# Kernel tuning notes

Measured on AMD Instinct MI355X. Metric: run time of the kernel, lower is better.

Reference implementation:

```python
import jax, jax.numpy as jnp
import numpy as np

N, C, K = 800_000, 64, 27  # active voxels, channels, 3^3 kernel offsets
EPS = 1e-5  # MinkowskiBatchNorm default eps


def setup_inputs() -> dict:
    key = jax.random.key(0)
    ks = jax.random.split(key, 9)
    x = jax.random.normal(ks[0], (N, C), jnp.float32)
    nbr = jax.random.randint(ks[1], (N, K), 0, N, jnp.int32)        # kernel-map input indices
    mask_bits = jax.random.randint(ks[2], (N, K), 0, 2, jnp.int32)
    W1 = jax.random.normal(ks[3], (K, C, C), jnp.float32) * 0.05    # conv1 weights (bias=False in ME)
    W2 = jax.random.normal(ks[4], (K, C, C), jnp.float32) * 0.05    # conv2 weights
    g1 = jax.random.normal(ks[5], (C,), jnp.float32) * 0.1 + 1.0
    b1 = jax.random.normal(ks[6], (C,), jnp.float32) * 0.1
    g2 = jax.random.normal(ks[7], (C,), jnp.float32) * 0.1 + 1.0
    b2 = jax.random.normal(ks[8], (C,), jnp.float32) * 0.1
    return {"x": x, "nbr": nbr, "mask_bits": mask_bits,
            "W1": W1, "g1": g1, "b1": b1, "W2": W2, "g2": g2, "b2": b2}


def _bn(h, gamma, beta):
    # training-mode BatchNorm over the point dimension (biased variance, as torch BN)
    mean = h.mean(axis=0)
    var = ((h - mean) ** 2).mean(axis=0)
    return (h - mean) * jax.lax.rsqrt(var + EPS) * gamma + beta


def _sparse_conv(h, nbr, mask, W):
    # gather-GEMM-scatter sparse conv: out[n] = sum_k mask[n,k] * h[nbr[n,k]] @ W[k]
    out0 = jnp.zeros((h.shape[0], W.shape[2]), h.dtype)

    def body(acc, kin):
        w_k, n_k, m_k = kin  # [C,C], [N], [N]
        acc = acc + (h[n_k] * m_k[:, None]) @ w_k
        return acc, None

    out, _ = jax.lax.scan(body, out0, (W, nbr.T, mask.T))
    return out


def reference(x, nbr, mask_bits, W1, g1, b1, W2, g2, b2):
    mask = mask_bits.astype(x.dtype)
    identity = x  # shortcut is identity: stride=1 and in_channels == out_channels
    out = jax.nn.relu(_bn(_sparse_conv(x, nbr, mask, W1), g1, b1))
    out = _bn(_sparse_conv(out, nbr, mask, W2), g2, b2)
    return jax.nn.relu(out + identity)
```

## Files before the change

### kernel.cpp

```cpp
#include <hip/hip_runtime.h>

typedef unsigned short u16;
typedef unsigned int u32;
typedef __bf16 bf16x8 __attribute__((ext_vector_type(8)));
typedef u16 u16x8 __attribute__((ext_vector_type(8)));
typedef float f32x4 __attribute__((ext_vector_type(4)));

#define KOFF 27
#define KPAD 28
#define EPSV 1e-5f
#define FRAGS_PER_CONV 14336
#define LDS_S 133

__device__ __forceinline__ u16 f2bf(float f) {
  u32 u = __builtin_bit_cast(u32, f);
  u = (u + 0x7FFFu + ((u >> 16) & 1u)) >> 16;
  return (u16)u;
}
__device__ __forceinline__ float bf2f(u16 h) {
  return __builtin_bit_cast(float, (u32)h << 16);
}

__device__ __forceinline__ void gl_lds16(const void* g, void* l) {
  __builtin_amdgcn_global_load_lds(
      (__attribute__((address_space(1))) void*)g,
      (__attribute__((address_space(3))) void*)l, 16, 0, 0);
}

__global__ void prep_x(const float* __restrict__ x, u16* __restrict__ xg, int n8) {
  int stride = gridDim.x * blockDim.x;
  for (int i = blockIdx.x * blockDim.x + threadIdx.x; i < n8; i += stride) {
    const f32x4* p = reinterpret_cast<const f32x4*>(x) + i * 2;
    f32x4 v0 = p[0], v1 = p[1];
    u16x8 o;
    o[0] = f2bf(v0[0]); o[1] = f2bf(v0[1]); o[2] = f2bf(v0[2]); o[3] = f2bf(v0[3]);
    o[4] = f2bf(v1[0]); o[5] = f2bf(v1[1]); o[6] = f2bf(v1[2]); o[7] = f2bf(v1[3]);
    reinterpret_cast<u16x8*>(xg)[i] = o;
  }
}

__global__ __launch_bounds__(256) void prep_tcidx(
    const int* __restrict__ nbr, const int* __restrict__ msk,
    int* __restrict__ cidx_q) {
  __shared__ int lds[27 * LDS_S + 16];
  const int tid = threadIdx.x;
  const int blk = blockIdx.x;
  const int in_base = blk * (128 * KOFF);
#pragma unroll
  for (int it = 0; it < 14; it++) {
    int t = tid + it * 256;
    if (t < 128 * KOFF) {
      int g = in_base + t;
      int v = msk[g] ? nbr[g] : -1;
      int row = (u32)t / KOFF;
      int k = t - row * KOFF;
      lds[k * LDS_S + row] = v;
    }
  }
  __syncthreads();
  const int out_base = blk * (2 * KPAD * 64);
#pragma unroll
  for (int it = 0; it < 14; it++) {
    int o = tid + it * 256;
    int q = (u32)o / (KPAD * 64);
    int rem = o - q * (KPAD * 64);
    int k = rem >> 6;
    int sub = rem & 63;
    int r = sub >> 2;
    int j = sub & 3;
    int v = (k < KOFF) ? lds[k * LDS_S + q * 64 + j * 16 + r] : -1;
    cidx_q[out_base + o] = v;
  }
}

__global__ void prep_w(const float* __restrict__ W1, const float* __restrict__ W2,
                       u16* __restrict__ wf) {
  int tid = blockIdx.x * blockDim.x + threadIdx.x;
  if (tid >= 2 * FRAGS_PER_CONV) return;
  int conv = tid / FRAGS_PER_CONV;
  int slot = tid - conv * FRAGS_PER_CONV;
  int k = slot >> 9;
  u16x8 o;
  if (k >= KOFF) {
#pragma unroll
    for (int j = 0; j < 8; j++) o[j] = 0;
  } else {
    const float* src = conv ? W2 : W1;
    int rest = slot & 511;
    int c = rest >> 8;
    int nt = (rest >> 6) & 3;
    int lane = rest & 63;
    int col = nt * 16 + (lane & 15);
    int kk0 = c * 32 + (lane >> 4) * 8;
    int base = k * 4096 + kk0 * 64 + col;
#pragma unroll
    for (int j = 0; j < 8; j++) o[j] = f2bf(src[base + j * 64]);
  }
  reinterpret_cast<u16x8*>(wf)[tid] = o;
}

__global__ __launch_bounds__(256, 4) void sconv(
    const u16* __restrict__ xg, const int* __restrict__ cidx_q,
    const u16* __restrict__ wf, u16* __restrict__ hout,
    float* __restrict__ psum, float* __restrict__ psq) {
  __shared__ __align__(1024) bf16x8 bsm[2][512];
  const int lane = threadIdx.x & 63;
  const int r = lane & 15;
  const int kg = lane >> 4;
  const int widInBlk = threadIdx.x >> 6;
  const int waveId = blockIdx.x * 4 + widInBlk;
  const char* wfc = (const char*)wf;
  const int chOff = kg * 8;
  bf16x8 zz;
#pragma unroll
  for (int j = 0; j < 8; j++) zz[j] = (__bf16)0.0f;

  const int n0 = waveId * 64;
  const int4* cpq = reinterpret_cast<const int4*>(cidx_q) +
                    (size_t)waveId * (KPAD * 16) + r;

  f32x4 acc[4][4];
#pragma unroll
  for (int j = 0; j < 4; j++)
#pragma unroll
    for (int nt = 0; nt < 4; nt++) {
      acc[j][nt][0] = 0.f; acc[j][nt][1] = 0.f;
      acc[j][nt][2] = 0.f; acc[j][nt][3] = 0.f;
    }

#define STAGEB(bc, ks)                                                     \
  {                                                                        \
    const char* s = wfc + ((size_t)(ks) << 13) + widInBlk * 1024 + lane * 16; \
    char* d = (char*)&bsm[bc][0] + widInBlk * 1024 + lane * 16;            \
    gl_lds16(s, d);                                                        \
    gl_lds16(s + 4096, d + 4096);                                          \
  }

  STAGEB(0, 0);

  for (int k = 0; k < KOFF; k++) {
    asm volatile("s_waitcnt vmcnt(0)" ::: "memory");
    __syncthreads();
    if (k + 1 < KOFF) STAGEB((k + 1) & 1, k + 1);

    int4 id4 = cpq[k << 4];
    bf16x8 a0[4], a1[4];
#pragma unroll
    for (int j = 0; j < 4; j++) { a0[j] = zz; a1[j] = zz; }
    if (id4.x >= 0) {
      const bf16x8* ap = reinterpret_cast<const bf16x8*>(xg + ((size_t)id4.x << 6) + chOff);
      a0[0] = ap[0]; a1[0] = ap[4];
    }
    if (id4.y >= 0) {
      const bf16x8* ap = reinterpret_cast<const bf16x8*>(xg + ((size_t)id4.y << 6) + chOff);
      a0[1] = ap[0]; a1[1] = ap[4];
    }
    if (id4.z >= 0) {
      const bf16x8* ap = reinterpret_cast<const bf16x8*>(xg + ((size_t)id4.z << 6) + chOff);
      a0[2] = ap[0]; a1[2] = ap[4];
    }
    if (id4.w >= 0) {
      const bf16x8* ap = reinterpret_cast<const bf16x8*>(xg + ((size_t)id4.w << 6) + chOff);
      a0[3] = ap[0]; a1[3] = ap[4];
    }
    const bf16x8* bl = &bsm[k & 1][0];
#pragma unroll
    for (int nt = 0; nt < 4; nt++) {
      bf16x8 b = bl[nt * 64 + lane];
#pragma unroll
      for (int j = 0; j < 4; j++)
        acc[j][nt] = __builtin_amdgcn_mfma_f32_16x16x32_bf16(a0[j], b, acc[j][nt], 0, 0, 0);
    }
#pragma unroll
    for (int nt = 0; nt < 4; nt++) {
      bf16x8 b = bl[256 + nt * 64 + lane];
#pragma unroll
      for (int j = 0; j < 4; j++)
        acc[j][nt] = __builtin_amdgcn_mfma_f32_16x16x32_bf16(a1[j], b, acc[j][nt], 0, 0, 0);
    }
  }
#undef STAGEB

  float ssum[4] = {0.f, 0.f, 0.f, 0.f};
  float ssq[4] = {0.f, 0.f, 0.f, 0.f};
#pragma unroll
  for (int j = 0; j < 4; j++) {
#pragma unroll
    for (int nt = 0; nt < 4; nt++) {
      const int col = nt * 16 + r;
      float rs = 0.f, rq = 0.f;
#pragma unroll
      for (int reg = 0; reg < 4; reg++) {
        float v = acc[j][nt][reg];
        rs += v;
        rq += v * v;
        hout[(size_t)(n0 + j * 16 + kg * 4 + reg) * 64 + col] = f2bf(v);
      }
      ssum[nt] += rs;
      ssq[nt] += rq;
    }
  }
#pragma unroll
  for (int nt = 0; nt < 4; nt++) {
    ssum[nt] += __shfl_xor(ssum[nt], 16, 64);
    ssum[nt] += __shfl_xor(ssum[nt], 32, 64);
    ssq[nt] += __shfl_xor(ssq[nt], 16, 64);
    ssq[nt] += __shfl_xor(ssq[nt], 32, 64);
  }
  if (lane < 16) {
#pragma unroll
    for (int nt = 0; nt < 4; nt++) {
      psum[(size_t)waveId * 64 + nt * 16 + lane] = ssum[nt];
      psq[(size_t)waveId * 64 + nt * 16 + lane] = ssq[nt];
    }
  }
}

__global__ void bn_finalize(const float* __restrict__ psum, const float* __restrict__ psq,
                            const float* __restrict__ g, const float* __restrict__ b,
                            float* __restrict__ scale, float* __restrict__ shift,
                            float invN, int nw) {
  int c = blockIdx.x;
  float s = 0.f, q = 0.f;
  for (int i = threadIdx.x; i < nw; i += blockDim.x) {
    s += psum[(size_t)i * 64 + c];
    q += psq[(size_t)i * 64 + c];
  }
#pragma unroll
  for (int off = 32; off >= 1; off >>= 1) {
    s += __shfl_down(s, off, 64);
    q += __shfl_down(q, off, 64);
  }
  __shared__ float ls[4], lq[4];
  int wid = threadIdx.x >> 6;
  int lane = threadIdx.x & 63;
  if (lane == 0) { ls[wid] = s; lq[wid] = q; }
  __syncthreads();
  if (threadIdx.x == 0) {
    s = ls[0] + ls[1] + ls[2] + ls[3];
    q = lq[0] + lq[1] + lq[2] + lq[3];
    float mean = s * invN;
    float var = q * invN - mean * mean;
    float rstd = rsqrtf(var + EPSV);
    float sc = rstd * g[c];
    scale[c] = sc;
    shift[c] = b[c] - mean * sc;
  }
}

__global__ void bn_relu_apply(const u16* __restrict__ h, const float* __restrict__ scale,
                              const float* __restrict__ shift, u16* __restrict__ y, int n8) {
  int i0 = blockIdx.x * blockDim.x + threadIdx.x;
  int c0 = (i0 * 8) & 63;
  float sc[8], sh[8];
#pragma unroll
  for (int j = 0; j < 8; j++) { sc[j] = scale[c0 + j]; sh[j] = shift[c0 + j]; }
  int stride = gridDim.x * blockDim.x;
  for (int i = i0; i < n8; i += stride) {
    u16x8 hv = reinterpret_cast<const u16x8*>(h)[i];
    u16x8 o;
#pragma unroll
    for (int j = 0; j < 8; j++) {
      float f = bf2f(hv[j]) * sc[j] + sh[j];
      o[j] = f2bf(fmaxf(f, 0.f));
    }
    reinterpret_cast<u16x8*>(y)[i] = o;
  }
}

__global__ void bn_add_relu(const u16* __restrict__ h, const float* __restrict__ scale,
                            const float* __restrict__ shift, const u16* __restrict__ xg,
                            float* __restrict__ out, int n8) {
  int i0 = blockIdx.x * blockDim.x + threadIdx.x;
  int c0 = (i0 * 8) & 63;
  float sc[8], sh[8];
#pragma unroll
  for (int j = 0; j < 8; j++) { sc[j] = scale[c0 + j]; sh[j] = shift[c0 + j]; }
  int stride = gridDim.x * blockDim.x;
  for (int i = i0; i < n8; i += stride) {
    u16x8 hv = reinterpret_cast<const u16x8*>(h)[i];
    u16x8 xv = reinterpret_cast<const u16x8*>(xg)[i];
    f32x4 o0, o1;
#pragma unroll
    for (int j = 0; j < 4; j++) {
      o0[j] = fmaxf(bf2f(hv[j]) * sc[j] + sh[j] + bf2f(xv[j]), 0.f);
      o1[j] = fmaxf(bf2f(hv[j + 4]) * sc[j + 4] + sh[j + 4] + bf2f(xv[j + 4]), 0.f);
    }
    f32x4* op = reinterpret_cast<f32x4*>(out) + i * 2;
    op[0] = o0;
    op[1] = o1;
  }
}

extern "C" void kernel_launch(void* const* d_in, const int* in_sizes, int n_in,
                              void* d_out, int out_size, void* d_ws, size_t ws_size,
                              hipStream_t stream) {
  const float* x = (const float*)d_in[0];
  const int* nbr = (const int*)d_in[1];
  const int* msk = (const int*)d_in[2];
  const float* W1 = (const float*)d_in[3];
  const float* g1 = (const float*)d_in[4];
  const float* b1 = (const float*)d_in[5];
  const float* W2 = (const float*)d_in[6];
  const float* g2 = (const float*)d_in[7];
  const float* b2 = (const float*)d_in[8];
  float* out = (float*)d_out;

  const int N = in_sizes[0] / 64;
  const int nquads = N / 64;
  const int nblocks = nquads / 4;
  const int n8 = N * 8;
  const size_t NC2 = (size_t)N * 64 * 2;
  const size_t MAPB = NC2 + 256;

  char* ws = (char*)d_ws;
  u16* bufA = (u16*)ws;
  u16* bufB = (u16*)(ws + MAPB);
  u16* wf = (u16*)(ws + 2 * MAPB);
  float* psum = (float*)(ws + 2 * MAPB + 512 * 1024);
  float* psq = psum + (size_t)nquads * 64;
  float* sc = psq + (size_t)nquads * 64;

  int* cidx_q = (int*)d_out;
  u16* y1 = (u16*)((char*)d_out + (size_t)N * KPAD * 4);

  float invN = 1.0f / (float)N;

  prep_x<<<2048, 256, 0, stream>>>(x, bufA, n8);
  prep_tcidx<<<N / 128, 256, 0, stream>>>(nbr, msk, cidx_q);
  prep_w<<<112, 256, 0, stream>>>(W1, W2, wf);
  sconv<<<nblocks, 256, 0, stream>>>(bufA, cidx_q, wf, bufB, psum, psq);
  bn_finalize<<<64, 256, 0, stream>>>(psum, psq, g1, b1, sc, sc + 64, invN, nquads);
  bn_relu_apply<<<2048, 256, 0, stream>>>(bufB, sc, sc + 64, y1, n8);
  sconv<<<nblocks, 256, 0, stream>>>(y1, cidx_q, wf + FRAGS_PER_CONV * 8, bufB, psum, psq);
  bn_finalize<<<64, 256, 0, stream>>>(psum, psq, g2, b2, sc + 128, sc + 192, invN, nquads);
  bn_add_relu<<<2048, 256, 0, stream>>>(bufB, sc + 128, sc + 192, bufA, out, n8);
}
```

Baseline: 841.1 us.

## Stage three kernel offsets per barrier with 512-thread sconv blocks

The sparse-conv kernel now uses 8-wave blocks and stages three offsets' weight fragments (24 KB) into LDS per phase, so the loop runs 10 barrier phases instead of 27. Weight fragments are padded to 30 slots and the grid is rounded up to whole 8-wave blocks. Waves past the last real row group still join the barriers but skip compute and write zero partial sums. The aim is to cut barrier and wait overhead per offset. In exchange the kernel uses more LDS per block, which may lower occupancy, and the padded waves do idle work.

```diff
diff --git a/kernel.cpp b/kernel.cpp
--- a/kernel.cpp
+++ b/kernel.cpp
@@ -8,8 +8,9 @@
 
 #define KOFF 27
 #define KPAD 28
+#define KSLOT 30
 #define EPSV 1e-5f
-#define FRAGS_PER_CONV 14336
+#define FRAGS_PER_CONV 15360
 #define LDS_S 133
 
 __device__ __forceinline__ u16 f2bf(float f) {
@@ -99,16 +100,17 @@
   reinterpret_cast<u16x8*>(wf)[tid] = o;
 }
 
-__global__ __launch_bounds__(256, 4) void sconv(
+__global__ __launch_bounds__(512, 4) void sconv(
     const u16* __restrict__ xg, const int* __restrict__ cidx_q,
     const u16* __restrict__ wf, u16* __restrict__ hout,
-    float* __restrict__ psum, float* __restrict__ psq) {
-  __shared__ __align__(1024) bf16x8 bsm[2][512];
+    float* __restrict__ psum, float* __restrict__ psq, int nquadsActive) {
+  __shared__ __align__(1024) bf16x8 bsm[2][1536];
   const int lane = threadIdx.x & 63;
   const int r = lane & 15;
   const int kg = lane >> 4;
   const int widInBlk = threadIdx.x >> 6;
-  const int waveId = blockIdx.x * 4 + widInBlk;
+  const int waveId = blockIdx.x * 8 + widInBlk;
+  const bool active = waveId < nquadsActive;
   const char* wfc = (const char*)wf;
   const int chOff = kg * 8;
   bf16x8 zz;
@@ -128,76 +130,85 @@
       acc[j][nt][2] = 0.f; acc[j][nt][3] = 0.f;
     }
 
-#define STAGEB(bc, ks)                                                     \
-  {                                                                        \
-    const char* s = wfc + ((size_t)(ks) << 13) + widInBlk * 1024 + lane * 16; \
-    char* d = (char*)&bsm[bc][0] + widInBlk * 1024 + lane * 16;            \
-    gl_lds16(s, d);                                                        \
-    gl_lds16(s + 4096, d + 4096);                                          \
-  }
-
-  STAGEB(0, 0);
-
-  for (int k = 0; k < KOFF; k++) {
+#define STAGE3(bc, ph)                                                        \
+  {                                                                           \
+    const char* s = wfc + (((size_t)(ph) * 3) << 13) + widInBlk * 1024 + lane * 16; \
+    char* d = (char*)&bsm[bc][0] + widInBlk * 1024 + lane * 16;               \
+    gl_lds16(s, d);                                                           \
+    gl_lds16(s + 8192, d + 8192);                                             \
+    gl_lds16(s + 16384, d + 16384);                                           \
+  }
+
+#define KSECT(K, bl)                                                          \
+  {                                                                           \
+    int4 id4 = cpq[(K) << 4];                                                 \
+    bf16x8 a0[4], a1[4];                                                      \
+    _Pragma("unroll") for (int j = 0; j < 4; j++) { a0[j] = zz; a1[j] = zz; } \
+    if (id4.x >= 0) {                                                         \
+      const bf16x8* ap = reinterpret_cast<const bf16x8*>(xg + ((size_t)id4.x << 6) + chOff); \
+      a0[0] = ap[0]; a1[0] = ap[4];                                           \
+    }                                                                         \
+    if (id4.y >= 0) {                                                         \
+      const bf16x8* ap = reinterpret_cast<const bf16x8*>(xg + ((size_t)id4.y << 6) + chOff); \
+      a0[1] = ap[0]; a1[1] = ap[4];                                           \
+    }                                                                         \
+    if (id4.z >= 0) {                                                         \
+      const bf16x8* ap = reinterpret_cast<const bf16x8*>(xg + ((size_t)id4.z << 6) + chOff); \
+      a0[2] = ap[0]; a1[2] = ap[4];                                           \
+    }                                                                         \
+    if (id4.w >= 0) {                                                         \
+      const bf16x8* ap = reinterpret_cast<const bf16x8*>(xg + ((size_t)id4.w << 6) + chOff); \
+      a0[3] = ap[0]; a1[3] = ap[4];                                           \
+    }                                                                         \
+    _Pragma("unroll") for (int nt = 0; nt < 4; nt++) {                        \
+      bf16x8 b = (bl)[nt * 64 + lane];                                        \
+      _Pragma("unroll") for (int j = 0; j < 4; j++)                           \
+        acc[j][nt] = __builtin_amdgcn_mfma_f32_16x16x32_bf16(a0[j], b, acc[j][nt], 0, 0, 0); \
+    }                                                                         \
+    _Pragma("unroll") for (int nt = 0; nt < 4; nt++) {                        \
+      bf16x8 b = (bl)[256 + nt * 64 + lane];                                  \
+      _Pragma("unroll") for (int j = 0; j < 4; j++)                           \
+        acc[j][nt] = __builtin_amdgcn_mfma_f32_16x16x32_bf16(a1[j], b, acc[j][nt], 0, 0, 0); \
+    }                                                                         \
+  }
+
+  STAGE3(0, 0);
+
+  for (int t = 0; t < 10; t++) {
     asm volatile("s_waitcnt vmcnt(0)" ::: "memory");
     __syncthreads();
-    if (k + 1 < KOFF) STAGEB((k + 1) & 1, k + 1);
-
-    int4 id4 = cpq[k << 4];
-    bf16x8 a0[4], a1[4];
-#pragma unroll
-    for (int j = 0; j < 4; j++) { a0[j] = zz; a1[j] = zz; }
-    if (id4.x >= 0) {
-      const bf16x8* ap = reinterpret_cast<const bf16x8*>(xg + ((size_t)id4.x << 6) + chOff);
-      a0[0] = ap[0]; a1[0] = ap[4];
-    }
-    if (id4.y >= 0) {
-      const bf16x8* ap = reinterpret_cast<const bf16x8*>(xg + ((size_t)id4.y << 6) + chOff);
-      a0[1] = ap[0]; a1[1] = ap[4];
-    }
-    if (id4.z >= 0) {
-      const bf16x8* ap = reinterpret_cast<const bf16x8*>(xg + ((size_t)id4.z << 6) + chOff);
-      a0[2] = ap[0]; a1[2] = ap[4];
-    }
-    if (id4.w >= 0) {
-      const bf16x8* ap = reinterpret_cast<const bf16x8*>(xg + ((size_t)id4.w << 6) + chOff);
-      a0[3] = ap[0]; a1[3] = ap[4];
-    }
-    const bf16x8* bl = &bsm[k & 1][0];
-#pragma unroll
-    for (int nt = 0; nt < 4; nt++) {
-      bf16x8 b = bl[nt * 64 + lane];
-#pragma unroll
-      for (int j = 0; j < 4; j++)
-        acc[j][nt] = __builtin_amdgcn_mfma_f32_16x16x32_bf16(a0[j], b, acc[j][nt], 0, 0, 0);
-    }
-#pragma unroll
-    for (int nt = 0; nt < 4; nt++) {
-      bf16x8 b = bl[256 + nt * 64 + lane];
-#pragma unroll
-      for (int j = 0; j < 4; j++)
-        acc[j][nt] = __builtin_amdgcn_mfma_f32_16x16x32_bf16(a1[j], b, acc[j][nt], 0, 0, 0);
-    }
-  }
-#undef STAGEB
+    if (t + 1 < 10) STAGE3((t + 1) & 1, t + 1);
+
+    if (active) {
+      const bf16x8* bl = &bsm[t & 1][0];
+      const int k0 = 3 * t;
+      KSECT(k0, bl);
+      if (k0 + 1 < KPAD) KSECT(k0 + 1, bl + 512);
+      if (k0 + 2 < KPAD) KSECT(k0 + 2, bl + 1024);
+    }
+  }
+#undef KSECT
+#undef STAGE3
 
   float ssum[4] = {0.f, 0.f, 0.f, 0.f};
   float ssq[4] = {0.f, 0.f, 0.f, 0.f};
-#pragma unroll
-  for (int j = 0; j < 4; j++) {
-#pragma unroll
-    for (int nt = 0; nt < 4; nt++) {
-      const int col = nt * 16 + r;
-      float rs = 0.f, rq = 0.f;
-#pragma unroll
-      for (int reg = 0; reg < 4; reg++) {
-        float v = acc[j][nt][reg];
-        rs += v;
-        rq += v * v;
-        hout[(size_t)(n0 + j * 16 + kg * 4 + reg) * 64 + col] = f2bf(v);
+  if (active) {
+#pragma unroll
+    for (int j = 0; j < 4; j++) {
+#pragma unroll
+      for (int nt = 0; nt < 4; nt++) {
+        const int col = nt * 16 + r;
+        float rs = 0.f, rq = 0.f;
+#pragma unroll
+        for (int reg = 0; reg < 4; reg++) {
+          float v = acc[j][nt][reg];
+          rs += v;
+          rq += v * v;
+          hout[(size_t)(n0 + j * 16 + kg * 4 + reg) * 64 + col] = f2bf(v);
+        }
+        ssum[nt] += rs;
+        ssq[nt] += rq;
       }
-      ssum[nt] += rs;
-      ssq[nt] += rq;
     }
   }
 #pragma unroll
@@ -308,7 +319,8 @@
 
   const int N = in_sizes[0] / 64;
   const int nquads = N / 64;
-  const int nblocks = nquads / 4;
+  const int nblocks = (nquads + 7) / 8;
+  const int nwslots = nblocks * 8;
   const int n8 = N * 8;
   const size_t NC2 = (size_t)N * 64 * 2;
   const size_t MAPB = NC2 + 256;
@@ -318,8 +330,8 @@
   u16* bufB = (u16*)(ws + MAPB);
   u16* wf = (u16*)(ws + 2 * MAPB);
   float* psum = (float*)(ws + 2 * MAPB + 512 * 1024);
-  float* psq = psum + (size_t)nquads * 64;
-  float* sc = psq + (size_t)nquads * 64;
+  float* psq = psum + (size_t)nwslots * 64;
+  float* sc = psq + (size_t)nwslots * 64;
 
   int* cidx_q = (int*)d_out;
   u16* y1 = (u16*)((char*)d_out + (size_t)N * KPAD * 4);
@@ -328,11 +340,11 @@
 
   prep_x<<<2048, 256, 0, stream>>>(x, bufA, n8);
   prep_tcidx<<<N / 128, 256, 0, stream>>>(nbr, msk, cidx_q);
-  prep_w<<<112, 256, 0, stream>>>(W1, W2, wf);
-  sconv<<<nblocks, 256, 0, stream>>>(bufA, cidx_q, wf, bufB, psum, psq);
-  bn_finalize<<<64, 256, 0, stream>>>(psum, psq, g1, b1, sc, sc + 64, invN, nquads);
+  prep_w<<<120, 256, 0, stream>>>(W1, W2, wf);
+  sconv<<<nblocks, 512, 0, stream>>>(bufA, cidx_q, wf, bufB, psum, psq, nquads);
+  bn_finalize<<<64, 256, 0, stream>>>(psum, psq, g1, b1, sc, sc + 64, invN, nwslots);
   bn_relu_apply<<<2048, 256, 0, stream>>>(bufB, sc, sc + 64, y1, n8);
-  sconv<<<nblocks, 256, 0, stream>>>(y1, cidx_q, wf + FRAGS_PER_CONV * 8, bufB, psum, psq);
-  bn_finalize<<<64, 256, 0, stream>>>(psum, psq, g2, b2, sc + 128, sc + 192, invN, nquads);
+  sconv<<<nblocks, 512, 0, stream>>>(y1, cidx_q, wf + FRAGS_PER_CONV * 8, bufB, psum, psq, nquads);
+  bn_finalize<<<64, 256, 0, stream>>>(psum, psq, g2, b2, sc + 128, sc + 192, invN, nwslots);
   bn_add_relu<<<2048, 256, 0, stream>>>(bufB, sc + 128, sc + 192, bufA, out, n8);
 }
```

After: 1.436 ms. 1.71x slower.
